# Performance work log

Measured on AMD Instinct MI355X. Metric: run time of the kernel, lower is better.

Reference implementation:

```python
import jax, jax.numpy as jnp
import numpy as np

B, L, D, H = 2, 1024, 1024, 16
HD = D // H  # head_dim = 64


def setup_inputs() -> dict:
    key = jax.random.key(0)
    ks = jax.random.split(key, 6)
    s = 1.0 / np.sqrt(D)
    return {
        "x": jax.random.normal(ks[0], (B, L, D), jnp.float32),
        "structure_bias": jax.random.normal(ks[1], (B, L, D), jnp.float32),
        # weights stored as [in, out] (transposed vs torch nn.Linear)
        "Wqkv": jax.random.normal(ks[2], (D, 3 * D), jnp.float32) * s,
        "bqkv": jnp.zeros((3 * D,), jnp.float32),
        "Ws": jax.random.normal(ks[3], (D, D), jnp.float32) * s,
        "bs": jnp.zeros((D,), jnp.float32),
        "Wo": jax.random.normal(ks[4], (D, D), jnp.float32) * s,
        "bo": jnp.zeros((D,), jnp.float32),
    }


def reference(x, structure_bias, Wqkv, bqkv, Ws, bs, Wo, bo):
    b, l, d = x.shape
    # qkv: [B, L, 3, H, HD] -> (3, B, H, L, HD)
    qkv = (x @ Wqkv + bqkv).reshape(b, l, 3, H, HD).transpose(2, 0, 3, 1, 4)
    q, k, v = qkv[0], qkv[1], qkv[2]
    scale = 1.0 / jnp.sqrt(jnp.float32(HD))
    attn = jnp.einsum("bhld,bhmd->bhlm", q, k) * scale  # [B,H,L,L]
    # structure bias: Linear then view(B, 1, L, L); requires L == feature_dim
    sw = (structure_bias @ Ws + bs).reshape(b, 1, l, l)
    attn = jax.nn.softmax(attn + sw, axis=-1)
    out = jnp.einsum("bhlm,bhmd->bhld", attn, v)  # [B,H,L,HD]
    out = out.transpose(0, 2, 1, 3).reshape(b, l, d)
    return out @ Wo + bo
```

## Files before the change

kernel.cpp:

```cpp
#include <hip/hip_runtime.h>
#include <stdint.h>
#include <stddef.h>


typedef float f32x4 __attribute__((ext_vector_type(4)));
typedef short s16x8 __attribute__((ext_vector_type(8)));
typedef unsigned short u16x8 __attribute__((ext_vector_type(8)));
typedef unsigned short u16x4 __attribute__((ext_vector_type(4)));

__device__ inline unsigned short f2bf(float f) {
    unsigned u = __builtin_bit_cast(unsigned, f);
    u += 0x7fffu + ((u >> 16) & 1u);
    return (unsigned short)(u >> 16);
}

__device__ inline f32x4 mfma16(s16x8 a, s16x8 b, f32x4 c) {
    return __builtin_amdgcn_mfma_f32_16x16x32_bf16(a, b, c, 0, 0, 0);
}

__device__ inline void gld_lds16(const void* g, const void* lds_base) {
    __builtin_amdgcn_global_load_lds(
        (const __attribute__((address_space(1))) void*)(uintptr_t)g,
        (__attribute__((address_space(3))) void*)(unsigned)(uintptr_t)lds_base,
        16, 0, 0);
}

__global__ __launch_bounds__(256) void prep_k(const float* __restrict__ x,
                                              const float* __restrict__ sb,
                                              const float* __restrict__ Wqkv,
                                              const float* __restrict__ Ws,
                                              const float* __restrict__ Wo,
                                              unsigned short* __restrict__ xb,
                                              unsigned short* __restrict__ sbb,
                                              unsigned short* __restrict__ wqkvt,
                                              unsigned short* __restrict__ wst,
                                              unsigned short* __restrict__ wot) {
    __shared__ float tile[64][65];
    const int blk = blockIdx.x, t = threadIdx.x;
    if (blk < 2048) {
        const float* src = (blk < 1024) ? x : sb;
        unsigned short* dst = (blk < 1024) ? xb : sbb;
        int i = (blk & 1023) * 256 + t;
        const float4* s4 = (const float4*)src;
        float4 a = s4[2 * i], b = s4[2 * i + 1];
        u16x8 o;
        o[0] = f2bf(a.x); o[1] = f2bf(a.y); o[2] = f2bf(a.z); o[3] = f2bf(a.w);
        o[4] = f2bf(b.x); o[5] = f2bf(b.y); o[6] = f2bf(b.z); o[7] = f2bf(b.w);
        *(u16x8*)(dst + (size_t)i * 8) = o;
        return;
    }
    int tt = blk - 2048;
    const float* W; unsigned short* Wt; int N, n0, k0;
    if (tt < 768)       { W = Wqkv; Wt = wqkvt; N = 3072; n0 = (tt % 48) * 64; k0 = (tt / 48) * 64; }
    else if (tt < 1024) { tt -= 768;  W = Ws; Wt = wst; N = 1024; n0 = (tt & 15) * 64; k0 = (tt >> 4) * 64; }
    else                { tt -= 1024; W = Wo; Wt = wot; N = 1024; n0 = (tt & 15) * 64; k0 = (tt >> 4) * 64; }
    const int lr = t >> 4, lc = (t & 15) * 4;
#pragma unroll
    for (int rr = 0; rr < 4; rr++) {
        int r = lr + rr * 16;
        float4 v = *(const float4*)(W + (size_t)(k0 + r) * N + n0 + lc);
        tile[r][lc] = v.x; tile[r][lc + 1] = v.y; tile[r][lc + 2] = v.z; tile[r][lc + 3] = v.w;
    }
    __syncthreads();
    const int wn = t >> 3, wk = (t & 7) * 8;
#pragma unroll
    for (int rr = 0; rr < 2; rr++) {
        int n = wn + rr * 32;
        u16x8 o;
#pragma unroll
        for (int j = 0; j < 8; j++) o[j] = f2bf(tile[wk + j][n]);
        *(u16x8*)(Wt + (size_t)(n0 + n) * 1024 + k0 + wk) = o;
    }
}

__global__ __launch_bounds__(256, 2) void gemm01_k(const unsigned short* __restrict__ xb,
                                                   const unsigned short* __restrict__ wqkvt,
                                                   const float* __restrict__ bqkv,
                                                   const unsigned short* __restrict__ sbb,
                                                   const unsigned short* __restrict__ wst,
                                                   const float* __restrict__ bs,
                                                   unsigned short* __restrict__ q,
                                                   unsigned short* __restrict__ kk_,
                                                   unsigned short* __restrict__ vt,
                                                   float* __restrict__ swf) {
    __shared__ unsigned short lA[2][8192];
    __shared__ unsigned short lB[2][8192];
    const int blk = blockIdx.x, t = threadIdx.x;
    const int wave = t >> 6, lane = t & 63, c = lane & 15, g = lane >> 4;
    const int wr = (wave >> 1) * 64, wc = (wave & 1) * 64;

    const unsigned short* A;
    const unsigned short* Bt;
    const float* bias;
    int bn0, bm0, epi;
    if (blk < 384) { A = xb;  Bt = wqkvt; bias = bqkv; epi = 0;
                     bn0 = (blk % 24) * 128; bm0 = (blk / 24) * 128; }
    else           { int bb = blk - 384; A = sbb; Bt = wst; bias = bs; epi = 1;
                     bn0 = (bb & 7) * 128; bm0 = (bb >> 3) * 128; }

    size_t aoff[4], boff[4];
#pragma unroll
    for (int j = 0; j < 4; j++) {
        int s = j * 256 + t, row = s >> 3, ch = (s & 7) ^ (row & 7);
        aoff[j] = (size_t)(bm0 + row) * 1024 + ch * 8;
        boff[j] = (size_t)(bn0 + row) * 1024 + ch * 8;
    }
    char* lAb0 = (char*)lA[0]; char* lBb0 = (char*)lB[0];

#define GS128(buf, kt)                                                                    \
    do {                                                                                  \
        _Pragma("unroll")                                                                 \
        for (int j = 0; j < 4; j++)                                                       \
            gld_lds16(A + aoff[j] + (kt), lAb0 + (buf) * 16384 + j * 4096 + wave * 1024); \
        _Pragma("unroll")                                                                 \
        for (int j = 0; j < 4; j++)                                                       \
            gld_lds16(Bt + boff[j] + (kt), lBb0 + (buf) * 16384 + j * 4096 + wave * 1024);\
    } while (0)

    f32x4 acc[4][4];
#pragma unroll
    for (int i = 0; i < 4; i++)
#pragma unroll
        for (int j = 0; j < 4; j++) acc[i][j] = {0.f, 0.f, 0.f, 0.f};

    GS128(0, 0);
    for (int ks = 0; ks < 16; ++ks) {
        __syncthreads();
        if (ks < 15) GS128((ks + 1) & 1, (ks + 1) * 64);
        const char* aB = lAb0 + (ks & 1) * 16384;
        const char* bB = lBb0 + (ks & 1) * 16384;
#pragma unroll
        for (int kk2 = 0; kk2 < 2; ++kk2) {
            s16x8 af[4], bfr[4];
#pragma unroll
            for (int i = 0; i < 4; i++) {
                int r_ = wr + i * 16 + c;
                af[i] = *(const s16x8*)(aB + r_ * 128 + (((kk2 * 4 + g) ^ (r_ & 7)) << 4));
            }
#pragma unroll
            for (int j = 0; j < 4; j++) {
                int r_ = wc + j * 16 + c;
                bfr[j] = *(const s16x8*)(bB + r_ * 128 + (((kk2 * 4 + g) ^ (r_ & 7)) << 4));
            }
            __builtin_amdgcn_s_setprio(1);
#pragma unroll
            for (int i = 0; i < 4; i++)
#pragma unroll
                for (int j = 0; j < 4; j++)
                    acc[i][j] = mfma16(af[i], bfr[j], acc[i][j]);
            __builtin_amdgcn_s_setprio(0);
        }
    }
#undef GS128

#pragma unroll
    for (int i = 0; i < 4; i++) {
#pragma unroll
        for (int j = 0; j < 4; j++) {
            const int n = bn0 + wc + j * 16 + c;
            const float bv = bias[n];
#pragma unroll
            for (int r = 0; r < 4; r++) {
                const int m = bm0 + wr + i * 16 + g * 4 + r;
                float v = acc[i][j][r] + bv;
                if (epi == 0) {
                    const int sel = n >> 10, h = (n >> 6) & 15, d = n & 63;
                    const int b_ = m >> 10, l_ = m & 1023;
                    const size_t bh = (size_t)((b_ << 4) + h);
                    unsigned short hv = f2bf(v);
                    if (sel == 0)      q[(bh * 1024 + l_) * 64 + d] = hv;
                    else if (sel == 1) kk_[(bh * 1024 + l_) * 64 + d] = hv;
                    else               vt[(bh * 64 + d) * 1024 + l_] = hv;
                } else {
                    swf[(size_t)m * 1024 + n] = v;
                }
            }
        }
    }
}

__global__ __launch_bounds__(256, 3) void gemmo_k(const unsigned short* __restrict__ A,
                                                  const unsigned short* __restrict__ Bt,
                                                  const float* __restrict__ bias,
                                                  float* __restrict__ outf) {
    __shared__ unsigned short lA[2][4096];
    __shared__ unsigned short lB[2][8192];
    const int t = threadIdx.x;
    const int wave = t >> 6, lane = t & 63, c = lane & 15, g = lane >> 4;
    const int bn0 = blockIdx.x * 128, bm0 = blockIdx.y * 64;
    const int wc = wave * 32;

    size_t aoff[2], boff[4];
#pragma unroll
    for (int j = 0; j < 2; j++) {
        int s = j * 256 + t, row = s >> 3, ch = (s & 7) ^ (row & 7);
        aoff[j] = (size_t)(bm0 + row) * 1024 + ch * 8;
    }
#pragma unroll
    for (int j = 0; j < 4; j++) {
        int s = j * 256 + t, row = s >> 3, ch = (s & 7) ^ (row & 7);
        boff[j] = (size_t)(bn0 + row) * 1024 + ch * 8;
    }
    char* lAb0 = (char*)lA[0]; char* lBb0 = (char*)lB[0];

#define GSTAGE(buf, kt)                                                                  \
    do {                                                                                 \
        _Pragma("unroll")                                                                \
        for (int j = 0; j < 2; j++)                                                      \
            gld_lds16(A + aoff[j] + (kt), lAb0 + (buf) * 8192 + j * 4096 + wave * 1024); \
        _Pragma("unroll")                                                                \
        for (int j = 0; j < 4; j++)                                                      \
            gld_lds16(Bt + boff[j] + (kt), lBb0 + (buf) * 16384 + j * 4096 + wave * 1024);\
    } while (0)

    f32x4 acc[4][2];
#pragma unroll
    for (int i = 0; i < 4; i++)
#pragma unroll
        for (int j = 0; j < 2; j++) acc[i][j] = {0.f, 0.f, 0.f, 0.f};

    GSTAGE(0, 0);
    for (int ks = 0; ks < 16; ++ks) {
        __syncthreads();
        if (ks < 15) GSTAGE((ks + 1) & 1, (ks + 1) * 64);
        const char* aB = lAb0 + (ks & 1) * 8192;
        const char* bB = lBb0 + (ks & 1) * 16384;
#pragma unroll
        for (int kk2 = 0; kk2 < 2; ++kk2) {
            s16x8 af[4], bfr[2];
#pragma unroll
            for (int i = 0; i < 4; i++) {
                int r_ = i * 16 + c;
                af[i] = *(const s16x8*)(aB + r_ * 128 + (((kk2 * 4 + g) ^ (r_ & 7)) << 4));
            }
#pragma unroll
            for (int j = 0; j < 2; j++) {
                int r_ = wc + j * 16 + c;
                bfr[j] = *(const s16x8*)(bB + r_ * 128 + (((kk2 * 4 + g) ^ (r_ & 7)) << 4));
            }
            __builtin_amdgcn_s_setprio(1);
#pragma unroll
            for (int i = 0; i < 4; i++)
#pragma unroll
                for (int j = 0; j < 2; j++)
                    acc[i][j] = mfma16(af[i], bfr[j], acc[i][j]);
            __builtin_amdgcn_s_setprio(0);
        }
    }
#undef GSTAGE

#pragma unroll
    for (int i = 0; i < 4; i++) {
#pragma unroll
        for (int j = 0; j < 2; j++) {
            const int n = bn0 + wc + j * 16 + c;
            const float bv = bias[n];
#pragma unroll
            for (int r = 0; r < 4; r++) {
                const int m = bm0 + i * 16 + g * 4 + r;
                outf[(size_t)m * 1024 + n] = acc[i][j][r] + bv;
            }
        }
    }
}

__global__ __launch_bounds__(512, 4) void attn_k(const unsigned short* __restrict__ q,
                                                 const unsigned short* __restrict__ k,
                                                 const unsigned short* __restrict__ vt,
                                                 const float* __restrict__ sw,
                                                 unsigned short* __restrict__ ctx) {
    __shared__ unsigned short kbuf[2][2][4096];
    __shared__ unsigned short vbuf[2][2][4096];
    const int t = threadIdx.x, wave = t >> 6, lane = t & 63, c = lane & 15, g = lane >> 4;
    const int grp = wave >> 2, wl = wave & 3;
    const int blk = blockIdx.x;
    const int qt = blk & 15, bh = blk >> 4, b_ = bh >> 4, h = bh & 15;
    const int qr = qt * 64 + wl * 16;

    const unsigned short* qbase = q + ((size_t)bh * 1024 + qr) * 64;
    s16x8 qf0 = *(const s16x8*)(qbase + (size_t)c * 64 + g * 8);
    s16x8 qf1 = *(const s16x8*)(qbase + (size_t)c * 64 + 32 + g * 8);

    const unsigned short* kg  = k + (size_t)bh * 65536 + (size_t)grp * 512 * 64;
    const unsigned short* vgb = vt + (size_t)bh * 65536 + grp * 512;
    const float* swrow = sw + ((size_t)b_ * 1024 + qr + c) * 1024 + grp * 512;

    const int s0 = wl * 128 + lane, s1 = s0 + 64;
    const int r0 = s0 >> 3, ch0 = (s0 & 7) ^ (r0 & 7) ^ (((r0 >> 3) & 1) << 2);
    const int r1 = s1 >> 3, ch1 = (s1 & 7) ^ (r1 & 7) ^ (((r1 >> 3) & 1) << 2);

    const float SC  = 0.125f * 1.4426950408889634f;
    const float L2E = 1.4426950408889634f;
    const float SHIFT = 16.0f;

    const short one_bf = (short)0x3F80;
    const s16x8 ones = { one_bf, one_bf, one_bf, one_bf, one_bf, one_bf, one_bf, one_bf };

    f32x4 acc[4];
    f32x4 accl = {0.f, 0.f, 0.f, 0.f};
#pragma unroll
    for (int nf = 0; nf < 4; nf++) acc[nf] = {0.f, 0.f, 0.f, 0.f};

    const int prm = ((c >> 2) << 3) | (c & 3);
    const int sz0 = (c & 3) ^ (((c >> 2) & 1) << 2);
    const int sz2 = sz0 ^ 4;
    const int swzv = (c & 7) ^ (((c >> 3) & 1) << 2);

    char* kgrp = (char*)kbuf + grp * 16384;
    char* vgrp = (char*)vbuf + grp * 16384;

#define STAGE(buf, kv0)                                                                     \
    do {                                                                                    \
        gld_lds16(kg + (size_t)((kv0) + r0) * 64 + ch0 * 8, kgrp + (buf) * 8192 + wl * 2048);          \
        gld_lds16(kg + (size_t)((kv0) + r1) * 64 + ch1 * 8, kgrp + (buf) * 8192 + wl * 2048 + 1024);   \
        gld_lds16(vgb + (size_t)r0 * 1024 + (kv0) + ch0 * 8, vgrp + (buf) * 8192 + wl * 2048);         \
        gld_lds16(vgb + (size_t)r1 * 1024 + (kv0) + ch1 * 8, vgrp + (buf) * 8192 + wl * 2048 + 1024);  \
    } while (0)

    STAGE(0, 0);
    __syncthreads();

    int cur = 0;
    for (int it = 0; it < 8; ++it) {
        const int kv0 = it * 64;
        if (it < 7) STAGE(cur ^ 1, kv0 + 64);

        const char* kB = kgrp + cur * 8192;
        const char* vB = vgrp + cur * 8192;
#pragma unroll
        for (int ks2 = 0; ks2 < 2; ++ks2) {
            float4 swa = *(const float4*)(swrow + kv0 + ks2 * 32 + 8 * g);
            float4 swb = *(const float4*)(swrow + kv0 + ks2 * 32 + 8 * g + 4);

            const int row0 = ks2 * 32 + prm;
            const int row2 = row0 + 4;
            s16x8 kc0 = *(const s16x8*)(kB + (row0 << 7) + (((0 + g) ^ sz0) << 4));
            s16x8 kc1 = *(const s16x8*)(kB + (row0 << 7) + (((4 + g) ^ sz0) << 4));
            s16x8 kc2 = *(const s16x8*)(kB + (row2 << 7) + (((0 + g) ^ sz2) << 4));
            s16x8 kc3 = *(const s16x8*)(kB + (row2 << 7) + (((4 + g) ^ sz2) << 4));

            __builtin_amdgcn_s_setprio(1);
            f32x4 ss0 = {0.f, 0.f, 0.f, 0.f}, ss1 = {0.f, 0.f, 0.f, 0.f};
            ss0 = mfma16(kc0, qf0, ss0); ss0 = mfma16(kc1, qf1, ss0);
            ss1 = mfma16(kc2, qf0, ss1); ss1 = mfma16(kc3, qf1, ss1);
            __builtin_amdgcn_s_setprio(0);

            s16x8 ap;
#pragma unroll
            for (int r = 0; r < 4; r++) {
                float z0 = ss0[r] * SC + ((&swa.x)[r] * L2E - SHIFT);
                float z1 = ss1[r] * SC + ((&swb.x)[r] * L2E - SHIFT);
                ap[r]     = (short)f2bf(__builtin_amdgcn_exp2f(z0));
                ap[4 + r] = (short)f2bf(__builtin_amdgcn_exp2f(z1));
            }

            __builtin_amdgcn_s_setprio(1);
            accl = mfma16(ones, ap, accl);
#pragma unroll
            for (int nf = 0; nf < 4; nf++) {
                s16x8 vf = *(const s16x8*)(vB + ((nf * 16 + c) << 7) + ((((ks2 << 2) + g) ^ swzv) << 4));
                acc[nf] = mfma16(vf, ap, acc[nf]);
            }
            __builtin_amdgcn_s_setprio(0);
        }
        __syncthreads();
        cur ^= 1;
    }
#undef STAGE

    float* pscr = (float*)vbuf;
    if (grp == 1) {
        float* pw = pscr + wl * 1040;
#pragma unroll
        for (int nf = 0; nf < 4; nf++)
#pragma unroll
            for (int r = 0; r < 4; r++)
                pw[(nf * 16 + 4 * g + r) * 16 + c] = acc[nf][r];
        if (g == 0) pw[1024 + c] = accl[0];
    }
    __syncthreads();

    float* scr = (float*)kbuf + wl * 1088;
    if (grp == 0) {
        float* pw = pscr + wl * 1040;
#pragma unroll
        for (int nf = 0; nf < 4; nf++)
#pragma unroll
            for (int r = 0; r < 4; r++)
                acc[nf][r] += pw[(nf * 16 + 4 * g + r) * 16 + c];
        float inv = 1.0f / (accl[0] + pw[1024 + c]);
#pragma unroll
        for (int nf = 0; nf < 4; nf++)
#pragma unroll
            for (int r = 0; r < 4; r++)
                scr[(nf * 16 + 4 * g + r) * 17 + c] = acc[nf][r] * inv;
    }
    __syncthreads();
    if (grp == 0) {
        u16x8 o0, o1;
#pragma unroll
        for (int j = 0; j < 8; j++) o0[j] = f2bf(scr[(g * 16 + j) * 17 + c]);
#pragma unroll
        for (int j = 0; j < 8; j++) o1[j] = f2bf(scr[(g * 16 + 8 + j) * 17 + c]);
        unsigned short* dst = ctx + ((size_t)(b_ << 10) + qr + c) * 1024 + (h << 6) + g * 16;
        *(u16x8*)dst = o0;
        *(u16x8*)(dst + 8) = o1;
    }
}

extern "C" void kernel_launch(void* const* d_in, const int* in_sizes, int n_in,
                              void* d_out, int out_size, void* d_ws, size_t ws_size,
                              hipStream_t stream) {
    const float* x    = (const float*)d_in[0];
    const float* sb   = (const float*)d_in[1];
    const float* Wqkv = (const float*)d_in[2];
    const float* bqkv = (const float*)d_in[3];
    const float* Ws   = (const float*)d_in[4];
    const float* bs   = (const float*)d_in[5];
    const float* Wo   = (const float*)d_in[6];
    const float* bo   = (const float*)d_in[7];
    float* out = (float*)d_out;

    char* ws = (char*)d_ws;
    unsigned short* xb    = (unsigned short*)(ws);
    unsigned short* sbb   = (unsigned short*)(ws + ((size_t)4 << 20));
    unsigned short* wqkvt = (unsigned short*)(ws + ((size_t)8 << 20));
    unsigned short* wst   = (unsigned short*)(ws + ((size_t)14 << 20));
    unsigned short* wot   = (unsigned short*)(ws + ((size_t)16 << 20));
    unsigned short* qb    = (unsigned short*)(ws + ((size_t)18 << 20));
    unsigned short* kb    = (unsigned short*)(ws + ((size_t)22 << 20));
    unsigned short* vtb   = (unsigned short*)(ws + ((size_t)26 << 20));
    float*          swf   = (float*)        (ws + ((size_t)30 << 20));
    unsigned short* ctxb  = (unsigned short*)(ws + ((size_t)38 << 20));

    prep_k<<<dim3(3328), dim3(256), 0, stream>>>(x, sb, Wqkv, Ws, Wo,
                                                 xb, sbb, wqkvt, wst, wot);
    gemm01_k<<<dim3(512), dim3(256), 0, stream>>>(xb, wqkvt, bqkv, sbb, wst, bs,
                                                  qb, kb, vtb, swf);
    attn_k<<<dim3(512), dim3(512), 0, stream>>>(qb, kb, vtb, swf, ctxb);
    gemmo_k<<<dim3(8, 32), dim3(256), 0, stream>>>(ctxb, wot, bo, out);
}
```

Baseline: 81.60 us.

## Store structure bias as bf16, remap block order for XCDs, retile output GEMM

The structure-bias projection is now written and read as bf16 instead of fp32, which halves the traffic of the large L×L bias matrix between the projection GEMM and attention, at some cost in precision. Block IDs in the GEMM and attention kernels are permuted so that consecutive blocks on the same XCD share operand tiles, aiming at better L2 reuse. The output GEMM is retiled from 64x128 to 64x64 tiles with 512 blocks and a 2x2 wave layout, trading per-block reuse for more parallelism.

After: 76.49 us. -6.3%, faster.

```diff
diff --git a/kernel.cpp b/kernel.cpp
--- a/kernel.cpp
+++ b/kernel.cpp
@@ -12,6 +12,9 @@
     unsigned u = __builtin_bit_cast(unsigned, f);
     u += 0x7fffu + ((u >> 16) & 1u);
     return (unsigned short)(u >> 16);
+}
+__device__ inline float bf2f(unsigned short h) {
+    return __builtin_bit_cast(float, (unsigned)h << 16);
 }
 
 __device__ inline f32x4 mfma16(s16x8 a, s16x8 b, f32x4 c) {
@@ -82,10 +85,11 @@
                                                    unsigned short* __restrict__ q,
                                                    unsigned short* __restrict__ kk_,
                                                    unsigned short* __restrict__ vt,
-                                                   float* __restrict__ swf) {
+                                                   unsigned short* __restrict__ swb) {
     __shared__ unsigned short lA[2][8192];
     __shared__ unsigned short lB[2][8192];
-    const int blk = blockIdx.x, t = threadIdx.x;
+    const int id = blockIdx.x, t = threadIdx.x;
+    const int blk = (id & 7) * 64 + (id >> 3);
     const int wave = t >> 6, lane = t & 63, c = lane & 15, g = lane >> 4;
     const int wr = (wave >> 1) * 64, wc = (wave & 1) * 64;
 
@@ -172,33 +176,30 @@
                     else if (sel == 1) kk_[(bh * 1024 + l_) * 64 + d] = hv;
                     else               vt[(bh * 64 + d) * 1024 + l_] = hv;
                 } else {
-                    swf[(size_t)m * 1024 + n] = v;
+                    swb[(size_t)m * 1024 + n] = f2bf(v);
                 }
             }
         }
     }
 }
 
-__global__ __launch_bounds__(256, 3) void gemmo_k(const unsigned short* __restrict__ A,
+__global__ __launch_bounds__(256, 2) void gemmo_k(const unsigned short* __restrict__ A,
                                                   const unsigned short* __restrict__ Bt,
                                                   const float* __restrict__ bias,
                                                   float* __restrict__ outf) {
     __shared__ unsigned short lA[2][4096];
-    __shared__ unsigned short lB[2][8192];
-    const int t = threadIdx.x;
+    __shared__ unsigned short lB[2][4096];
+    const int id = blockIdx.x, t = threadIdx.x;
+    const int blk = (id & 7) * 64 + (id >> 3);
     const int wave = t >> 6, lane = t & 63, c = lane & 15, g = lane >> 4;
-    const int bn0 = blockIdx.x * 128, bm0 = blockIdx.y * 64;
-    const int wc = wave * 32;
-
-    size_t aoff[2], boff[4];
+    const int bn0 = (blk & 15) * 64, bm0 = (blk >> 4) * 64;
+    const int wr = (wave >> 1) * 32, wc = (wave & 1) * 32;
+
+    size_t aoff[2], boff[2];
 #pragma unroll
     for (int j = 0; j < 2; j++) {
         int s = j * 256 + t, row = s >> 3, ch = (s & 7) ^ (row & 7);
         aoff[j] = (size_t)(bm0 + row) * 1024 + ch * 8;
-    }
-#pragma unroll
-    for (int j = 0; j < 4; j++) {
-        int s = j * 256 + t, row = s >> 3, ch = (s & 7) ^ (row & 7);
         boff[j] = (size_t)(bn0 + row) * 1024 + ch * 8;
     }
     char* lAb0 = (char*)lA[0]; char* lBb0 = (char*)lB[0];
@@ -209,13 +210,13 @@
         for (int j = 0; j < 2; j++)                                                      \
             gld_lds16(A + aoff[j] + (kt), lAb0 + (buf) * 8192 + j * 4096 + wave * 1024); \
         _Pragma("unroll")                                                                \
-        for (int j = 0; j < 4; j++)                                                      \
-            gld_lds16(Bt + boff[j] + (kt), lBb0 + (buf) * 16384 + j * 4096 + wave * 1024);\
+        for (int j = 0; j < 2; j++)                                                      \
+            gld_lds16(Bt + boff[j] + (kt), lBb0 + (buf) * 8192 + j * 4096 + wave * 1024);\
     } while (0)
 
-    f32x4 acc[4][2];
-#pragma unroll
-    for (int i = 0; i < 4; i++)
+    f32x4 acc[2][2];
+#pragma unroll
+    for (int i = 0; i < 2; i++)
 #pragma unroll
         for (int j = 0; j < 2; j++) acc[i][j] = {0.f, 0.f, 0.f, 0.f};
 
@@ -224,13 +225,13 @@
         __syncthreads();
         if (ks < 15) GSTAGE((ks + 1) & 1, (ks + 1) * 64);
         const char* aB = lAb0 + (ks & 1) * 8192;
-        const char* bB = lBb0 + (ks & 1) * 16384;
+        const char* bB = lBb0 + (ks & 1) * 8192;
 #pragma unroll
         for (int kk2 = 0; kk2 < 2; ++kk2) {
-            s16x8 af[4], bfr[2];
-#pragma unroll
-            for (int i = 0; i < 4; i++) {
-                int r_ = i * 16 + c;
+            s16x8 af[2], bfr[2];
+#pragma unroll
+            for (int i = 0; i < 2; i++) {
+                int r_ = wr + i * 16 + c;
                 af[i] = *(const s16x8*)(aB + r_ * 128 + (((kk2 * 4 + g) ^ (r_ & 7)) << 4));
             }
 #pragma unroll
@@ -240,7 +241,7 @@
             }
             __builtin_amdgcn_s_setprio(1);
 #pragma unroll
-            for (int i = 0; i < 4; i++)
+            for (int i = 0; i < 2; i++)
 #pragma unroll
                 for (int j = 0; j < 2; j++)
                     acc[i][j] = mfma16(af[i], bfr[j], acc[i][j]);
@@ -250,14 +251,14 @@
 #undef GSTAGE
 
 #pragma unroll
-    for (int i = 0; i < 4; i++) {
+    for (int i = 0; i < 2; i++) {
 #pragma unroll
         for (int j = 0; j < 2; j++) {
             const int n = bn0 + wc + j * 16 + c;
             const float bv = bias[n];
 #pragma unroll
             for (int r = 0; r < 4; r++) {
-                const int m = bm0 + i * 16 + g * 4 + r;
+                const int m = bm0 + wr + i * 16 + g * 4 + r;
                 outf[(size_t)m * 1024 + n] = acc[i][j][r] + bv;
             }
         }
@@ -267,14 +268,18 @@
 __global__ __launch_bounds__(512, 4) void attn_k(const unsigned short* __restrict__ q,
                                                  const unsigned short* __restrict__ k,
                                                  const unsigned short* __restrict__ vt,
-                                                 const float* __restrict__ sw,
+                                                 const unsigned short* __restrict__ sw,
                                                  unsigned short* __restrict__ ctx) {
     __shared__ unsigned short kbuf[2][2][4096];
     __shared__ unsigned short vbuf[2][2][4096];
     const int t = threadIdx.x, wave = t >> 6, lane = t & 63, c = lane & 15, g = lane >> 4;
     const int grp = wave >> 2, wl = wave & 3;
-    const int blk = blockIdx.x;
-    const int qt = blk & 15, bh = blk >> 4, b_ = bh >> 4, h = bh & 15;
+    const int id = blockIdx.x;
+    const int pos = id >> 3;
+    const int group = (id & 7) * 4 + (pos >> 4);
+    const int h = pos & 15;
+    const int b_ = group >> 4, qt = group & 15;
+    const int bh = b_ * 16 + h;
     const int qr = qt * 64 + wl * 16;
 
     const unsigned short* qbase = q + ((size_t)bh * 1024 + qr) * 64;
@@ -283,7 +288,7 @@
 
     const unsigned short* kg  = k + (size_t)bh * 65536 + (size_t)grp * 512 * 64;
     const unsigned short* vgb = vt + (size_t)bh * 65536 + grp * 512;
-    const float* swrow = sw + ((size_t)b_ * 1024 + qr + c) * 1024 + grp * 512;
+    const unsigned short* swrow = sw + ((size_t)b_ * 1024 + qr + c) * 1024 + grp * 512;
 
     const int s0 = wl * 128 + lane, s1 = s0 + 64;
     const int r0 = s0 >> 3, ch0 = (s0 & 7) ^ (r0 & 7) ^ (((r0 >> 3) & 1) << 2);
@@ -329,8 +334,7 @@
         const char* vB = vgrp + cur * 8192;
 #pragma unroll
         for (int ks2 = 0; ks2 < 2; ++ks2) {
-            float4 swa = *(const float4*)(swrow + kv0 + ks2 * 32 + 8 * g);
-            float4 swb = *(const float4*)(swrow + kv0 + ks2 * 32 + 8 * g + 4);
+            u16x8 swv = *(const u16x8*)(swrow + kv0 + ks2 * 32 + 8 * g);
 
             const int row0 = ks2 * 32 + prm;
             const int row2 = row0 + 4;
@@ -348,8 +352,8 @@
             s16x8 ap;
 #pragma unroll
             for (int r = 0; r < 4; r++) {
-                float z0 = ss0[r] * SC + ((&swa.x)[r] * L2E - SHIFT);
-                float z1 = ss1[r] * SC + ((&swb.x)[r] * L2E - SHIFT);
+                float z0 = ss0[r] * SC + (bf2f(swv[r]) * L2E - SHIFT);
+                float z1 = ss1[r] * SC + (bf2f(swv[4 + r]) * L2E - SHIFT);
                 ap[r]     = (short)f2bf(__builtin_amdgcn_exp2f(z0));
                 ap[4 + r] = (short)f2bf(__builtin_amdgcn_exp2f(z1));
             }
@@ -430,13 +434,13 @@
     unsigned short* qb    = (unsigned short*)(ws + ((size_t)18 << 20));
     unsigned short* kb    = (unsigned short*)(ws + ((size_t)22 << 20));
     unsigned short* vtb   = (unsigned short*)(ws + ((size_t)26 << 20));
-    float*          swf   = (float*)        (ws + ((size_t)30 << 20));
+    unsigned short* swbuf = (unsigned short*)(ws + ((size_t)30 << 20));
     unsigned short* ctxb  = (unsigned short*)(ws + ((size_t)38 << 20));
 
     prep_k<<<dim3(3328), dim3(256), 0, stream>>>(x, sb, Wqkv, Ws, Wo,
                                                  xb, sbb, wqkvt, wst, wot);
     gemm01_k<<<dim3(512), dim3(256), 0, stream>>>(xb, wqkvt, bqkv, sbb, wst, bs,
-                                                  qb, kb, vtb, swf);
-    attn_k<<<dim3(512), dim3(512), 0, stream>>>(qb, kb, vtb, swf, ctxb);
-    gemmo_k<<<dim3(8, 32), dim3(256), 0, stream>>>(ctxb, wot, bo, out);
-}
+                                                  qb, kb, vtb, swbuf);
+    attn_k<<<dim3(512), dim3(512), 0, stream>>>(qb, kb, vtb, swbuf, ctxb);
+    gemmo_k<<<dim3(512), dim3(256), 0, stream>>>(ctxb, wot, bo, out);
+}
```
